# Optimization experiments

Measured on AMD Instinct MI355X. Metric: run time of the kernel, lower is better.

## Reference

```python
import jax, jax.numpy as jnp
import numpy as np

N_NODES = 50000
N_EDGES = 800000
IN_DIM = 128
EDGE_DIM = 64
OUT_DIM = 128


def setup_inputs() -> dict:
    key = jax.random.key(0)
    ks = jax.random.split(key, 9)
    nfeat = jax.random.normal(ks[0], (N_NODES, IN_DIM), dtype=jnp.float32)
    efeat = jax.random.normal(ks[1], (N_EDGES, EDGE_DIM), dtype=jnp.float32)
    src = jax.random.randint(ks[2], (N_EDGES,), 0, N_NODES, dtype=jnp.int32)
    dst = jax.random.randint(ks[3], (N_EDGES,), 0, N_NODES, dtype=jnp.int32)
    # learned params (Kaiming-ish scaling)
    W_edge = jax.random.normal(ks[4], (EDGE_DIM, OUT_DIM), dtype=jnp.float32) / np.float32(np.sqrt(EDGE_DIM))
    W_ne = jax.random.normal(ks[5], (IN_DIM + OUT_DIM, OUT_DIM), dtype=jnp.float32) / np.float32(np.sqrt(IN_DIM + OUT_DIM))
    b_ne = jnp.zeros((OUT_DIM,), dtype=jnp.float32)
    W_self = jax.random.normal(ks[6], (IN_DIM, OUT_DIM), dtype=jnp.float32) / np.float32(np.sqrt(IN_DIM))
    b_self = jnp.zeros((OUT_DIM,), dtype=jnp.float32)
    return {"nfeat": nfeat, "efeat": efeat, "src": src, "dst": dst,
            "W_edge": W_edge, "W_ne": W_ne, "b_ne": b_ne,
            "W_self": W_self, "b_self": b_self}


def reference(nfeat, efeat, src, dst, W_edge, W_ne, b_ne, W_self, b_self):
    # per-edge message: relu(Linear(concat(src_h, edge_map(efeat))))
    eh = efeat @ W_edge                      # [E, OUT]
    src_h = nfeat[src]                        # [E, IN]  (gather)
    # split-matmul form of concat([src_h, eh]) @ W_ne (identical math, no concat buffer)
    m = jax.nn.relu(src_h @ W_ne[:IN_DIM] + eh @ W_ne[IN_DIM:] + b_ne)  # [E, OUT]
    # segment-mean scatter by destination node (dgl.function.mean -> 0 for isolated nodes)
    summ = jax.ops.segment_sum(m, dst, num_segments=N_NODES)             # [N, OUT]
    cnt = jax.ops.segment_sum(jnp.ones((m.shape[0], 1), m.dtype), dst, num_segments=N_NODES)
    neigh = summ / jnp.maximum(cnt, 1.0)
    # self transform
    out = neigh + nfeat @ W_self + b_self
    return out
```

## Files before the change

kernel.cpp:

```cpp
#include <hip/hip_runtime.h>

#define N_NODES 50000
#define N_EDGES 800000
#define IN_DIM  128
#define EDGE_DIM 64
#define OUT_DIM 128
#define NTILES  (N_EDGES / 128)
#define NODE_TILES ((N_NODES + 127) / 128)
#define W2_BLOCKS 32
#define ZERO_BLOCKS 196

typedef __attribute__((ext_vector_type(8))) short bf16x8;
typedef __attribute__((ext_vector_type(4))) float f32x4;
typedef unsigned short u16;

__device__ __forceinline__ u16 f2bf(float f) {
    union { float f; unsigned u; } x; x.f = f;
    unsigned r = x.u + 0x7FFFu + ((x.u >> 16) & 1u);
    return (u16)(r >> 16);
}
__device__ __forceinline__ float bf2f(u16 h) {
    union { unsigned u; float f; } x; x.u = ((unsigned)h) << 16;
    return x.f;
}
__device__ __forceinline__ bf16x8 pack8(const float* v) {
    bf16x8 r;
#pragma unroll
    for (int i = 0; i < 8; ++i) r[i] = (short)f2bf(v[i]);
    return r;
}

__global__ __launch_bounds__(256, 1) void prep_kernel(
    const float* __restrict__ nfeat, const float* __restrict__ W_ne,
    const float* __restrict__ W_self, const float* __restrict__ b_self,
    const float* __restrict__ W_edge,
    u16* __restrict__ H1, u16* __restrict__ HS,
    float* __restrict__ W2fT, int* __restrict__ cnts) {

    __shared__ __align__(16) char Nb[128 * 128 * 2];

    const int bid = blockIdx.x;
    const int tid = threadIdx.x;

    if (bid >= NODE_TILES) {
        if (bid < NODE_TILES + W2_BLOCKS) {
            const int idx = (bid - NODE_TILES) * 256 + tid;
            const int c = idx >> 7;
            const int o = idx & 127;
            float acc = 0.0f;
            for (int i = 0; i < OUT_DIM; ++i)
                acc += W_edge[c * OUT_DIM + i] * W_ne[(IN_DIM + i) * OUT_DIM + o];
            W2fT[o * EDGE_DIM + c] = acc;
        } else {
            const int i = (bid - NODE_TILES - W2_BLOCKS) * 256 + tid;
            if (i < N_NODES) cnts[i] = 0;
        }
        return;
    }

    const int w    = tid >> 6;
    const int l    = tid & 63;
    const int lrow = l & 15;
    const int lq   = l >> 4;

    const bool isSelf = (w >= 2);
    const float* W = isSelf ? W_self : W_ne;
    const int colw = (w & 1) * 64;
    u16* Y = isSelf ? HS : H1;

    bf16x8 Wf[4][4];
#pragma unroll
    for (int mt = 0; mt < 4; ++mt) {
        const int c = colw + mt * 16 + lrow;
#pragma unroll
        for (int kk = 0; kk < 4; ++kk) {
            float tmp[8];
#pragma unroll
            for (int t = 0; t < 8; ++t) tmp[t] = W[(kk * 32 + lq * 8 + t) * 128 + c];
            Wf[mt][kk] = pack8(tmp);
        }
    }
    float4 bias4[4];
#pragma unroll
    for (int mt = 0; mt < 4; ++mt) {
        if (isSelf) bias4[mt] = *(const float4*)(b_self + colw + mt * 16 + lq * 4);
        else { bias4[mt].x = 0.f; bias4[mt].y = 0.f; bias4[mt].z = 0.f; bias4[mt].w = 0.f; }
    }

    const int srow = tid >> 1;
    const int skc  = (tid & 1) * 8;
    const int r0 = bid * 128;
    {
        const int gr = min(r0 + srow, N_NODES - 1);
        const float4* np = (const float4*)(nfeat + (size_t)gr * 128 + skc * 8);
        const int swz = (srow & 7);
#pragma unroll
        for (int j = 0; j < 8; ++j) {
            float4 x = np[2 * j], y = np[2 * j + 1];
            float tmp[8] = {x.x, x.y, x.z, x.w, y.x, y.y, y.z, y.w};
            bf16x8 f = pack8(tmp);
            const int kc = skc + j;
            *(bf16x8*)(Nb + srow * 256 + (((kc) ^ swz) * 16)) = f;
        }
    }
    __syncthreads();

    f32x4 acc[4][8];
#pragma unroll
    for (int mt = 0; mt < 4; ++mt)
#pragma unroll
        for (int nt = 0; nt < 8; ++nt) {
            acc[mt][nt][0] = bias4[mt].x; acc[mt][nt][1] = bias4[mt].y;
            acc[mt][nt][2] = bias4[mt].z; acc[mt][nt][3] = bias4[mt].w;
        }
#pragma unroll
    for (int nt = 0; nt < 8; ++nt) {
        const int r = nt * 16 + lrow;
        const int swz = (r & 7);
        bf16x8 Be[4];
#pragma unroll
        for (int kk = 0; kk < 4; ++kk)
            Be[kk] = *(const bf16x8*)(Nb + r * 256 + (((kk * 4 + lq) ^ swz) * 16));
#pragma unroll
        for (int mt = 0; mt < 4; ++mt)
#pragma unroll
            for (int kk = 0; kk < 4; ++kk)
                acc[mt][nt] = __builtin_amdgcn_mfma_f32_16x16x32_bf16(Wf[mt][kk], Be[kk], acc[mt][nt], 0, 0, 0);
    }

#pragma unroll
    for (int nt = 0; nt < 8; ++nt) {
        const int n = r0 + nt * 16 + lrow;
        if (n < N_NODES) {
#pragma unroll
            for (int mt = 0; mt < 4; ++mt) {
                const int c0 = colw + mt * 16 + lq * 4;
                ushort4 o;
                o.x = f2bf(acc[mt][nt][0]); o.y = f2bf(acc[mt][nt][1]);
                o.z = f2bf(acc[mt][nt][2]); o.w = f2bf(acc[mt][nt][3]);
                *(ushort4*)(Y + (size_t)n * 128 + c0) = o;
            }
        }
    }
}

__global__ void count_rank_kernel(const int* __restrict__ dst,
                                  int* __restrict__ counts, int* __restrict__ rank) {
    const int e = blockIdx.x * blockDim.x + threadIdx.x;
    if (e < N_EDGES) rank[e] = atomicAdd(&counts[dst[e]], 1);
}

#define SCAN_T 1024
#define SCAN_CHUNK 49
__global__ void scan_kernel(const int* __restrict__ counts, int* __restrict__ off) {
    __shared__ int part[SCAN_T];
    const int t = threadIdx.x;
    const int base = t * SCAN_CHUNK;
    int s = 0;
    for (int k = 0; k < SCAN_CHUNK; ++k) {
        const int i = base + k;
        if (i < N_NODES) s += counts[i];
    }
    part[t] = s;
    __syncthreads();
    for (int d = 1; d < SCAN_T; d <<= 1) {
        int v = (t >= d) ? part[t - d] : 0;
        __syncthreads();
        part[t] += v;
        __syncthreads();
    }
    int excl = part[t] - s;
    for (int k = 0; k < SCAN_CHUNK; ++k) {
        const int i = base + k;
        if (i < N_NODES) { off[i] = excl; excl += counts[i]; }
    }
    if (t == SCAN_T - 1) off[N_NODES] = excl;
}

__global__ __launch_bounds__(256, 3) void edge_gemm_scatter_kernel(
    const float* __restrict__ efeat, const int* __restrict__ src,
    const int* __restrict__ dst, const int* __restrict__ rank,
    const int* __restrict__ offs, const float* __restrict__ W2fT,
    const float* __restrict__ b_ne, const u16* __restrict__ H1,
    u16* __restrict__ mbuf) {

    __shared__ __align__(16) char Ab[128 * 64 * 2];
    __shared__ int sS[128];
    __shared__ int sT[128];

    const int tid  = threadIdx.x;
    const int w    = tid >> 6;
    const int l    = tid & 63;
    const int lrow = l & 15;
    const int lq   = l >> 4;

    bf16x8 Wf[2][2];
    float4 bias4[2];
#pragma unroll
    for (int mt = 0; mt < 2; ++mt) {
        const int c = w * 32 + mt * 16 + lrow;
#pragma unroll
        for (int kk = 0; kk < 2; ++kk) {
            const float* wp = W2fT + c * 64 + kk * 32 + lq * 8;
            float tmp[8];
#pragma unroll
            for (int j = 0; j < 8; ++j) tmp[j] = wp[j];
            Wf[mt][kk] = pack8(tmp);
        }
        bias4[mt] = *(const float4*)(b_ne + w * 32 + mt * 16 + lq * 4);
    }

    const int srow = tid >> 1;
    const int skh  = (tid & 1) * 32;

    for (int tile = blockIdx.x; tile < NTILES; tile += gridDim.x) {
        const int e0 = tile * 128;

        if (tid < 128) {
            const int e = e0 + tid;
            sS[tid] = src[e];
            sT[tid] = offs[dst[e]] + rank[e];
        }
        {
            const float4* ep = (const float4*)(efeat + (size_t)(e0 + srow) * 64 + skh);
            const int swz = (srow & 7) << 4;
#pragma unroll
            for (int j = 0; j < 4; ++j) {
                float4 x = ep[2 * j], y = ep[2 * j + 1];
                float tmp[8] = {x.x, x.y, x.z, x.w, y.x, y.y, y.z, y.w};
                bf16x8 f = pack8(tmp);
                *(bf16x8*)(Ab + ((srow * 128 + skh * 2 + j * 16) ^ swz)) = f;
            }
        }
        __syncthreads();

        f32x4 acc[2][8];
#pragma unroll
        for (int mt = 0; mt < 2; ++mt)
#pragma unroll
            for (int nt = 0; nt < 8; ++nt) {
                acc[mt][nt][0] = bias4[mt].x; acc[mt][nt][1] = bias4[mt].y;
                acc[mt][nt][2] = bias4[mt].z; acc[mt][nt][3] = bias4[mt].w;
            }
#pragma unroll
        for (int nt = 0; nt < 8; ++nt) {
            const int r = nt * 16 + lrow;
            const int swz = (r & 7) << 4;
            bf16x8 Be0 = *(const bf16x8*)(Ab + ((r * 128 + lq * 16) ^ swz));
            bf16x8 Be1 = *(const bf16x8*)(Ab + ((r * 128 + 64 + lq * 16) ^ swz));
#pragma unroll
            for (int mt = 0; mt < 2; ++mt) {
                acc[mt][nt] = __builtin_amdgcn_mfma_f32_16x16x32_bf16(Wf[mt][0], Be0, acc[mt][nt], 0, 0, 0);
                acc[mt][nt] = __builtin_amdgcn_mfma_f32_16x16x32_bf16(Wf[mt][1], Be1, acc[mt][nt], 0, 0, 0);
            }
        }

#pragma unroll
        for (int nt = 0; nt < 8; ++nt) {
            const int e  = nt * 16 + lrow;
            const int sn = sS[e];
            const int st = sT[e];
#pragma unroll
            for (int mt = 0; mt < 2; ++mt) {
                const int c0 = w * 32 + mt * 16 + lq * 4;
                ushort4 h4 = *(const ushort4*)(H1 + (size_t)sn * 128 + c0);
                ushort4 o;
                o.x = f2bf(fmaxf(acc[mt][nt][0] + bf2f(h4.x), 0.0f));
                o.y = f2bf(fmaxf(acc[mt][nt][1] + bf2f(h4.y), 0.0f));
                o.z = f2bf(fmaxf(acc[mt][nt][2] + bf2f(h4.z), 0.0f));
                o.w = f2bf(fmaxf(acc[mt][nt][3] + bf2f(h4.w), 0.0f));
                *(ushort4*)(mbuf + (size_t)st * 128 + c0) = o;
            }
        }
        __syncthreads();
    }
}

__global__ __launch_bounds__(256, 4) void reduce_kernel(
    const int* __restrict__ off, const u16* __restrict__ mbuf,
    const u16* __restrict__ HS, float* __restrict__ out) {
    const int n = (blockIdx.x * blockDim.x + threadIdx.x) >> 6;
    if (n >= N_NODES) return;
    const int l  = threadIdx.x & 63;
    const int cs = l & 7;
    const int rg = l >> 3;
    const int s0 = off[n], s1 = off[n + 1];

    float facc[16];
#pragma unroll
    for (int i = 0; i < 16; ++i) facc[i] = 0.0f;
    for (int s = s0 + rg; s < s1; s += 8) {
        const u16* rp = mbuf + (size_t)s * 128 + cs * 16;
        bf16x8 v0 = *(const bf16x8*)(rp);
        bf16x8 v1 = *(const bf16x8*)(rp + 8);
#pragma unroll
        for (int i = 0; i < 8; ++i) {
            facc[i]     += bf2f((u16)v0[i]);
            facc[i + 8] += bf2f((u16)v1[i]);
        }
    }
#pragma unroll
    for (int i = 0; i < 16; ++i) {
        facc[i] += __shfl_xor(facc[i], 8, 64);
        facc[i] += __shfl_xor(facc[i], 16, 64);
        facc[i] += __shfl_xor(facc[i], 32, 64);
    }
    if (rg == 0) {
        const int c = s1 - s0;
        const float inv = (c > 0) ? 1.0f / (float)c : 0.0f;
        const u16* hp = HS + (size_t)n * 128 + cs * 16;
        bf16x8 h0 = *(const bf16x8*)(hp);
        bf16x8 h1 = *(const bf16x8*)(hp + 8);
        float r[16];
#pragma unroll
        for (int i = 0; i < 8; ++i) {
            r[i]     = facc[i]     * inv + bf2f((u16)h0[i]);
            r[i + 8] = facc[i + 8] * inv + bf2f((u16)h1[i]);
        }
        float* op = out + (size_t)n * 128 + cs * 16;
#pragma unroll
        for (int q = 0; q < 4; ++q) {
            float4 o4;
            o4.x = r[q * 4 + 0]; o4.y = r[q * 4 + 1];
            o4.z = r[q * 4 + 2]; o4.w = r[q * 4 + 3];
            *(float4*)(op + q * 4) = o4;
        }
    }
}

extern "C" void kernel_launch(void* const* d_in, const int* in_sizes, int n_in,
                              void* d_out, int out_size, void* d_ws, size_t ws_size,
                              hipStream_t stream) {
    const float* nfeat  = (const float*)d_in[0];
    const float* efeat  = (const float*)d_in[1];
    const int*   src    = (const int*)d_in[2];
    const int*   dst    = (const int*)d_in[3];
    const float* W_edge = (const float*)d_in[4];
    const float* W_ne   = (const float*)d_in[5];
    const float* b_ne   = (const float*)d_in[6];
    const float* W_self = (const float*)d_in[7];
    const float* b_self = (const float*)d_in[8];

    float* out = (float*)d_out;
    char* ws = (char*)d_ws;

    const size_t OFF_W2   = 0;
    const size_t OFF_CNT  = 32768;
    const size_t OFF_OFFS = 232960;
    const size_t OFF_RANK = 433152;
    const size_t OFF_H1   = 3633152;
    const size_t OFF_HS   = 16433152;
    const size_t OFF_M    = 29233152;

    float* W2fT = (float*)(ws + OFF_W2);
    int*   cnts = (int*)(ws + OFF_CNT);
    int*   offs = (int*)(ws + OFF_OFFS);
    int*   rank = (int*)(ws + OFF_RANK);
    u16*   H1   = (u16*)(ws + OFF_H1);
    u16*   HS   = (u16*)(ws + OFF_HS);
    u16*   mbuf = (u16*)(ws + OFF_M);

    prep_kernel<<<NODE_TILES + W2_BLOCKS + ZERO_BLOCKS, 256, 0, stream>>>(
        nfeat, W_ne, W_self, b_self, W_edge, H1, HS, W2fT, cnts);
    count_rank_kernel<<<(N_EDGES + 255) / 256, 256, 0, stream>>>(dst, cnts, rank);
    scan_kernel<<<1, SCAN_T, 0, stream>>>(cnts, offs);
    edge_gemm_scatter_kernel<<<2048, 256, 0, stream>>>(
        efeat, src, dst, rank, offs, W2fT, b_ne, H1, mbuf);
    reduce_kernel<<<(N_NODES * 64 + 255) / 256, 256, 0, stream>>>(offs, mbuf, HS, out);
}
```

Before: 354.6 us.

## Stage H1 gather and message scatter through LDS with full-row vector accesses

```diff
diff --git a/kernel.cpp b/kernel.cpp
--- a/kernel.cpp
+++ b/kernel.cpp
@@ -8,7 +8,7 @@
 #define NTILES  (N_EDGES / 128)
 #define NODE_TILES ((N_NODES + 127) / 128)
 #define W2_BLOCKS 32
-#define ZERO_BLOCKS 196
+#define CNT_BLOCKS ((N_EDGES + 255) / 256)
 
 typedef __attribute__((ext_vector_type(8))) short bf16x8;
 typedef __attribute__((ext_vector_type(4))) float f32x4;
@@ -29,13 +29,16 @@
     for (int i = 0; i < 8; ++i) r[i] = (short)f2bf(v[i]);
     return r;
 }
+__device__ __forceinline__ int hswz(int r, int chunk) {
+    return r * 256 + ((chunk ^ ((((r & 7) ^ ((r >> 3) & 7))) << 2)) * 8);
+}
 
 __global__ __launch_bounds__(256, 1) void prep_kernel(
     const float* __restrict__ nfeat, const float* __restrict__ W_ne,
     const float* __restrict__ W_self, const float* __restrict__ b_self,
-    const float* __restrict__ W_edge,
+    const float* __restrict__ W_edge, const int* __restrict__ dst,
     u16* __restrict__ H1, u16* __restrict__ HS,
-    float* __restrict__ W2fT, int* __restrict__ cnts) {
+    float* __restrict__ W2fT, int* __restrict__ cnts, int* __restrict__ rank) {
 
     __shared__ __align__(16) char Nb[128 * 128 * 2];
 
@@ -52,8 +55,8 @@
                 acc += W_edge[c * OUT_DIM + i] * W_ne[(IN_DIM + i) * OUT_DIM + o];
             W2fT[o * EDGE_DIM + c] = acc;
         } else {
-            const int i = (bid - NODE_TILES - W2_BLOCKS) * 256 + tid;
-            if (i < N_NODES) cnts[i] = 0;
+            const int e = (bid - NODE_TILES - W2_BLOCKS) * 256 + tid;
+            if (e < N_EDGES) rank[e] = atomicAdd(&cnts[dst[e]], 1);
         }
         return;
     }
@@ -142,12 +145,6 @@
             }
         }
     }
-}
-
-__global__ void count_rank_kernel(const int* __restrict__ dst,
-                                  int* __restrict__ counts, int* __restrict__ rank) {
-    const int e = blockIdx.x * blockDim.x + threadIdx.x;
-    if (e < N_EDGES) rank[e] = atomicAdd(&counts[dst[e]], 1);
 }
 
 #define SCAN_T 1024
@@ -185,6 +182,7 @@
     u16* __restrict__ mbuf) {
 
     __shared__ __align__(16) char Ab[128 * 64 * 2];
+    __shared__ __align__(16) char HMb[128 * 128 * 2];
     __shared__ int sS[128];
     __shared__ int sT[128];
 
@@ -193,6 +191,8 @@
     const int l    = tid & 63;
     const int lrow = l & 15;
     const int lq   = l >> 4;
+    const int g    = tid >> 4;
+    const int gi   = tid & 15;
 
     bf16x8 Wf[2][2];
     float4 bias4[2];
@@ -234,6 +234,13 @@
         }
         __syncthreads();
 
+        bf16x8 hreg[8];
+#pragma unroll
+        for (int k = 0; k < 8; ++k) {
+            const int r = g * 8 + k;
+            hreg[k] = *(const bf16x8*)(H1 + (size_t)sS[r] * 128 + gi * 8);
+        }
+
         f32x4 acc[2][8];
 #pragma unroll
         for (int mt = 0; mt < 2; ++mt)
@@ -256,23 +263,37 @@
         }
 
 #pragma unroll
+        for (int k = 0; k < 8; ++k) {
+            const int r = g * 8 + k;
+            *(bf16x8*)(HMb + hswz(r, 2 * gi)) = hreg[k];
+        }
+        __syncthreads();
+
+#pragma unroll
         for (int nt = 0; nt < 8; ++nt) {
-            const int e  = nt * 16 + lrow;
-            const int sn = sS[e];
-            const int st = sT[e];
+            const int e = nt * 16 + lrow;
 #pragma unroll
             for (int mt = 0; mt < 2; ++mt) {
                 const int c0 = w * 32 + mt * 16 + lq * 4;
-                ushort4 h4 = *(const ushort4*)(H1 + (size_t)sn * 128 + c0);
+                const int byte = hswz(e, c0 >> 2);
+                ushort4 h4 = *(const ushort4*)(HMb + byte);
                 ushort4 o;
                 o.x = f2bf(fmaxf(acc[mt][nt][0] + bf2f(h4.x), 0.0f));
                 o.y = f2bf(fmaxf(acc[mt][nt][1] + bf2f(h4.y), 0.0f));
                 o.z = f2bf(fmaxf(acc[mt][nt][2] + bf2f(h4.z), 0.0f));
                 o.w = f2bf(fmaxf(acc[mt][nt][3] + bf2f(h4.w), 0.0f));
-                *(ushort4*)(mbuf + (size_t)st * 128 + c0) = o;
-            }
-        }
-        __syncthreads();
+                *(ushort4*)(HMb + byte) = o;
+            }
+        }
+        __syncthreads();
+
+#pragma unroll
+        for (int k = 0; k < 8; ++k) {
+            const int r  = g * 8 + k;
+            const int st = sT[r];
+            bf16x8 v = *(const bf16x8*)(HMb + hswz(r, 2 * gi));
+            *(bf16x8*)(mbuf + (size_t)st * 128 + gi * 8) = v;
+        }
     }
 }
 
@@ -360,9 +381,9 @@
     u16*   HS   = (u16*)(ws + OFF_HS);
     u16*   mbuf = (u16*)(ws + OFF_M);
 
-    prep_kernel<<<NODE_TILES + W2_BLOCKS + ZERO_BLOCKS, 256, 0, stream>>>(
-        nfeat, W_ne, W_self, b_self, W_edge, H1, HS, W2fT, cnts);
-    count_rank_kernel<<<(N_EDGES + 255) / 256, 256, 0, stream>>>(dst, cnts, rank);
+    hipMemsetAsync(cnts, 0, N_NODES * sizeof(int), stream);
+    prep_kernel<<<NODE_TILES + W2_BLOCKS + CNT_BLOCKS, 256, 0, stream>>>(
+        nfeat, W_ne, W_self, b_self, W_edge, dst, H1, HS, W2fT, cnts, rank);
     scan_kernel<<<1, SCAN_T, 0, stream>>>(cnts, offs);
     edge_gemm_scatter_kernel<<<2048, 256, 0, stream>>>(
         efeat, src, dst, rank, offs, W2fT, b_ne, H1, mbuf);
```

Result: faster. 302.6 us (-14.7%).
